# Performance work log

Measured on AMD Instinct MI355X. Metric: run time of the kernel, lower is better.

The kernel has to match this reference:

```python
import jax, jax.numpy as jnp
import numpy as np

B, C_IN, C_OUT, STYLE_DIM, H, W = 8, 512, 512, 512, 32, 32

def setup_inputs() -> dict:
    key = jax.random.key(0)
    k = jax.random.split(key, 7)
    x = jax.random.normal(k[0], (B, C_IN, H, W), dtype=jnp.float32)
    style = jax.random.normal(k[1], (B, STYLE_DIM), dtype=jnp.float32)
    noise = jax.random.normal(k[2], (B, 1, 2 * H, 2 * W), dtype=jnp.float32)
    # learned params (Conv2d weight, style_fc Linear, output bias)
    conv_w = jax.random.normal(k[3], (C_OUT, C_IN, 3, 3), dtype=jnp.float32) * 0.05
    fc_w = jax.random.normal(k[4], (C_IN, STYLE_DIM), dtype=jnp.float32) * 0.05
    fc_b = jax.random.normal(k[5], (C_IN,), dtype=jnp.float32) * 0.05
    bias = jnp.zeros((1, C_OUT, 1, 1), dtype=jnp.float32)
    return {"x": x, "style": style, "noise": noise,
            "conv_w": conv_w, "fc_w": fc_w, "fc_b": fc_b, "bias": bias}

def reference(x, style, noise, conv_w, fc_w, fc_b, bias):
    b, c, h, w = x.shape
    o = conv_w.shape[0]
    x = jnp.repeat(jnp.repeat(x, 2, axis=2), 2, axis=3)  # (B, C, 2H, 2W)
    # style modulation: (B, C)
    s = style @ fc_w.T + fc_b
    # per-sample modulated weight (B, O, C, 3, 3)
    wmod = conv_w[None] * (s[:, None, :, None, None] + 1.0)
    # demodulation
    d = jax.lax.rsqrt(jnp.sum(wmod * wmod, axis=(2, 3, 4)) + 1e-8)  # (B, O)
    wmod = wmod * d[:, :, None, None, None]
    # grouped conv: one group per batch sample
    xr = x.reshape(1, b * c, 2 * h, 2 * w)
    wr = wmod.reshape(b * o, c, 3, 3)
    y = jax.lax.conv_general_dilated(
        xr, wr, window_strides=(1, 1), padding='SAME',
        feature_group_count=b,
        dimension_numbers=('NCHW', 'OIHW', 'NCHW'))
    y = y.reshape(b, o, 2 * h, 2 * w) + bias + noise
    return jax.nn.leaky_relu(y, negative_slope=0.2)
```

## Files before the change

### kernel.cpp

```cpp
#include <hip/hip_runtime.h>

typedef short v8s __attribute__((ext_vector_type(8)));
typedef float f32x4 __attribute__((ext_vector_type(4)));
typedef unsigned short ushort_t;

#define BB    8
#define CIN   512
#define COUT  512
#define SDIM  512

static __device__ __forceinline__ ushort_t f2bf(float f) {
    union { float f; unsigned u; } un; un.f = f;
    unsigned r = un.u + 0x7FFF + ((un.u >> 16) & 1);
    return (ushort_t)(r >> 16);
}

__global__ void k_style(const float* __restrict__ style, const float* __restrict__ fc_w,
                        const float* __restrict__ fc_b, float* __restrict__ m) {
    __shared__ float sst[SDIM];
    const int b = blockIdx.y;
    for (int k = threadIdx.x; k < SDIM; k += 256) sst[k] = style[b * SDIM + k];
    __syncthreads();
    const int c = blockIdx.x * 256 + threadIdx.x;
    float acc = fc_b[c];
    const float* wr = fc_w + c * SDIM;
    for (int k = 0; k < SDIM; k += 4) {
        float4 w4 = *(const float4*)(wr + k);
        acc += w4.x * sst[k] + w4.y * sst[k + 1] + w4.z * sst[k + 2] + w4.w * sst[k + 3];
    }
    m[b * CIN + c] = acc + 1.0f;
}

__global__ void k_wprep(const float* __restrict__ conv_w, float* __restrict__ q,
                        ushort_t* __restrict__ Wb) {
    const int idx = blockIdx.x * 256 + threadIdx.x;
    if (idx >= COUT * CIN) return;
    const int o = idx >> 9, c = idx & 511;
    float w[3][3];
    const float* wp = conv_w + idx * 9;
    float qs = 0.f;
    for (int i = 0; i < 3; i++)
        for (int j = 0; j < 3; j++) {
            float v = wp[i * 3 + j];
            w[i][j] = v;
            qs += v * v;
        }
    q[idx] = qs;
    const int ch = c >> 5, kg = (c >> 3) & 3, c8 = c & 7;
    for (int py = 0; py < 2; py++) {
        float rs[2][3];
        for (int kx = 0; kx < 3; kx++) {
            rs[0][kx] = (py == 0) ? w[0][kx] : w[0][kx] + w[1][kx];
            rs[1][kx] = (py == 0) ? w[1][kx] + w[2][kx] : w[2][kx];
        }
        for (int px = 0; px < 2; px++) {
            const int p = py * 2 + px;
            float vals[4];
            if (px == 0) {
                vals[0] = rs[0][0];
                vals[1] = rs[0][1] + rs[0][2];
                vals[2] = rs[1][0];
                vals[3] = rs[1][1] + rs[1][2];
            } else {
                vals[0] = rs[0][0] + rs[0][1];
                vals[1] = rs[0][2];
                vals[2] = rs[1][0] + rs[1][1];
                vals[3] = rs[1][2];
            }
            for (int t = 0; t < 4; t++)
                Wb[(size_t)p * (16 * 4 * 4 * 512 * 8) + (size_t)ch * (4 * 4 * 512 * 8)
                   + ((size_t)(t * 4 + kg) * 512 + o) * 8 + c8] = f2bf(vals[t]);
        }
    }
}

__global__ void k_demod(const float* __restrict__ m, const float* __restrict__ q,
                        float* __restrict__ d) {
    const int w = (blockIdx.x * 256 + threadIdx.x) >> 6;
    const int L = threadIdx.x & 63;
    const int b = w >> 9, o = w & 511;
    float4 q1 = *(const float4*)(q + o * 512 + L * 8);
    float4 q2 = *(const float4*)(q + o * 512 + L * 8 + 4);
    float4 m1 = *(const float4*)(m + b * 512 + L * 8);
    float4 m2 = *(const float4*)(m + b * 512 + L * 8 + 4);
    float acc = m1.x * m1.x * q1.x + m1.y * m1.y * q1.y + m1.z * m1.z * q1.z +
                m1.w * m1.w * q1.w + m2.x * m2.x * q2.x + m2.y * m2.y * q2.y +
                m2.z * m2.z * q2.z + m2.w * m2.w * q2.w;
    for (int off = 32; off; off >>= 1) acc += __shfl_down(acc, off, 64);
    if (L == 0) d[w] = rsqrtf(acc + 1e-8f);
}

__global__ void k_xprep(const float* __restrict__ x, const float* __restrict__ m,
                        ushort_t* __restrict__ Xt) {
    __shared__ __align__(16) ushort_t lt[32 * 528];
    const int r = blockIdx.x, b = blockIdx.y, t = threadIdx.x;
    for (int s = t; s < 4096; s += 256) {
        const int c = s >> 3, q4 = (s & 7) * 4;
        float4 v = *(const float4*)(x + (((size_t)(b * CIN + c) * 32 + r) * 32 + q4));
        const float mv = m[b * CIN + c];
        lt[(q4 + 0) * 528 + c] = f2bf(v.x * mv);
        lt[(q4 + 1) * 528 + c] = f2bf(v.y * mv);
        lt[(q4 + 2) * 528 + c] = f2bf(v.z * mv);
        lt[(q4 + 3) * 528 + c] = f2bf(v.w * mv);
    }
    __syncthreads();
    for (int s = t; s < 2048; s += 256) {
        const int qq = s >> 6, c8 = s & 63;
        v8s v = *(v8s*)&lt[qq * 528 + c8 * 8];
        *(v8s*)(Xt + (((size_t)(b * 32 + r) * 32 + qq) * 512 + c8 * 8)) = v;
    }
}

#define KS 136

__global__ __launch_bounds__(256, 2) void k_gemm(
    const ushort_t* __restrict__ Xt, const ushort_t* __restrict__ Wb,
    const float* __restrict__ dmod, const float* __restrict__ bias,
    const float* __restrict__ noise, float* __restrict__ out) {
    __shared__ __align__(16) ushort_t Wt[128 * KS];
    __shared__ __align__(16) ushort_t Xs[128 * KS];

    const int tid = threadIdx.x;
    const int L = tid & 63, wid = tid >> 6;
    const int o0 = blockIdx.x * 128;
    const int r0 = blockIdx.y * 4;
    const int b = blockIdx.z >> 2, p = blockIdx.z & 3;
    const int py = p >> 1, px = p & 1;
    const int ry0 = py ? 0 : -1, cx0 = px ? 0 : -1;
    const int wo = (wid >> 1) * 64, wn = (wid & 1) * 64;
    const int l15 = L & 15, l4 = L >> 4;

    const ushort_t* XtB = Xt + (size_t)b * (32 * 32 * 512);
    const ushort_t* WbP = Wb + (size_t)p * (16 * 4 * 4 * 512 * 8);
    const v8s z8 = {0, 0, 0, 0, 0, 0, 0, 0};

    f32x4 acc[4][4];
#pragma unroll
    for (int i = 0; i < 4; i++)
#pragma unroll
        for (int j = 0; j < 4; j++) acc[i][j] = {0.f, 0.f, 0.f, 0.f};

    v8s rw[8], rx[8];

    auto loadc = [&](int c0) {
        const ushort_t* WbC = WbP + (size_t)(c0 >> 5) * (4 * 4 * 512 * 8);
#pragma unroll
        for (int i = 0; i < 8; i++) {
            const int slot = tid + i * 256;
            const int row = slot >> 4, t = (slot >> 2) & 3, cg = slot & 3;
            rw[i] = *(const v8s*)(WbC + ((size_t)((t * 4 + cg) * 512 + o0 + row)) * 8);
            const int gr = r0 + (row >> 5) + ry0 + (t >> 1);
            const int gq = (row & 31) + cx0 + (t & 1);
            v8s xv = z8;
            if ((unsigned)gr < 32u && (unsigned)gq < 32u)
                xv = *(const v8s*)(XtB + (size_t)((gr * 32 + gq) * 512 + c0 + cg * 8));
            rx[i] = xv;
        }
    };

    loadc(0);
    for (int c0 = 0; c0 < CIN; c0 += 32) {
        __syncthreads();
#pragma unroll
        for (int i = 0; i < 8; i++) {
            const int slot = tid + i * 256;
            const int row = slot >> 4, t = (slot >> 2) & 3, cg = slot & 3;
            const int ldso = row * KS + t * 32 + cg * 8;
            *(v8s*)&Wt[ldso] = rw[i];
            *(v8s*)&Xs[ldso] = rx[i];
        }
        __syncthreads();
        if (c0 + 32 < CIN) loadc(c0 + 32);
#pragma unroll
        for (int s = 0; s < 4; s++) {
            const int kb = s * 32 + l4 * 8;
            v8s af[4], bf[4];
#pragma unroll
            for (int i = 0; i < 4; i++)
                af[i] = *(const v8s*)&Wt[(wo + i * 16 + l15) * KS + kb];
#pragma unroll
            for (int j = 0; j < 4; j++)
                bf[j] = *(const v8s*)&Xs[(wn + j * 16 + l15) * KS + kb];
#pragma unroll
            for (int i = 0; i < 4; i++)
#pragma unroll
                for (int j = 0; j < 4; j++)
                    acc[i][j] = __builtin_amdgcn_mfma_f32_16x16x32_bf16(
                        af[i], bf[j], acc[i][j], 0, 0, 0);
        }
    }

    const float* db = dmod + b * COUT;
    float nz[4];
    int ooff[4];
#pragma unroll
    for (int j = 0; j < 4; j++) {
        const int n = wn + j * 16 + l15;
        const int Y = 2 * (r0 + (n >> 5)) + py, X = 2 * (n & 31) + px;
        nz[j] = noise[b * 4096 + Y * 64 + X];
        ooff[j] = Y * 64 + X;
    }
    float* outB = out + (size_t)b * COUT * 4096;
#pragma unroll
    for (int i = 0; i < 4; i++) {
        const int ob = o0 + wo + i * 16 + l4 * 4;
        float4 d4 = *(const float4*)(db + ob);
        float4 b4 = *(const float4*)(bias + ob);
        const float dv[4] = {d4.x, d4.y, d4.z, d4.w};
        const float bv[4] = {b4.x, b4.y, b4.z, b4.w};
#pragma unroll
        for (int reg = 0; reg < 4; reg++) {
            float* orow = outB + (size_t)(ob + reg) * 4096;
#pragma unroll
            for (int j = 0; j < 4; j++) {
                float v = acc[i][j][reg] * dv[reg] + bv[reg] + nz[j];
                orow[ooff[j]] = v > 0.f ? v : 0.2f * v;
            }
        }
    }
}

extern "C" void kernel_launch(void* const* d_in, const int* in_sizes, int n_in,
                              void* d_out, int out_size, void* d_ws, size_t ws_size,
                              hipStream_t stream) {
    const float* x      = (const float*)d_in[0];
    const float* style  = (const float*)d_in[1];
    const float* noise  = (const float*)d_in[2];
    const float* conv_w = (const float*)d_in[3];
    const float* fc_w   = (const float*)d_in[4];
    const float* fc_b   = (const float*)d_in[5];
    const float* bias   = (const float*)d_in[6];
    float* out = (float*)d_out;

    float* ws = (float*)d_ws;
    float* m    = ws;
    float* dmod = ws + 4096;
    float* q    = ws + 8192;
    ushort_t* XtU = (ushort_t*)(ws + 270336);
    ushort_t* WbU = XtU + 4194304;

    k_style<<<dim3(2, BB), 256, 0, stream>>>(style, fc_w, fc_b, m);
    k_wprep<<<(COUT * CIN + 255) / 256, 256, 0, stream>>>(conv_w, q, WbU);
    k_xprep<<<dim3(32, BB), 256, 0, stream>>>(x, m, XtU);
    k_demod<<<1024, 256, 0, stream>>>(m, q, dmod);
    k_gemm<<<dim3(4, 8, 32), 256, 0, stream>>>(XtU, WbU, dmod, bias, noise, out);
}
```

Measured before the change: 215.1 us.

## Merge prep kernels and double-buffer GEMM with direct global-to-LDS loads

Fuses the four preprocessing kernels into two launches, which removes launch overhead and serialization. The GEMM main loop now uses global_load_lds to copy tiles straight into double-buffered, XOR-swizzled LDS, replacing the register-staged single buffer and stepping K by 16 channels with one barrier per step. Out-of-range halo loads read from a zeroed guard buffer. Block indices are remapped to change the scheduling order across CUs. The new scheme depends on global_load_lds wave-slot layout semantics and adds more loop iterations.

```diff
diff --git a/kernel.cpp b/kernel.cpp
--- a/kernel.cpp
+++ b/kernel.cpp
@@ -9,122 +9,136 @@
 #define COUT  512
 #define SDIM  512
 
+#define GLDS(g, l)                                                      \
+    __builtin_amdgcn_global_load_lds(                                   \
+        (const __attribute__((address_space(1))) void*)(g),             \
+        (__attribute__((address_space(3))) void*)(l), 16, 0, 0)
+
 static __device__ __forceinline__ ushort_t f2bf(float f) {
     union { float f; unsigned u; } un; un.f = f;
     unsigned r = un.u + 0x7FFF + ((un.u >> 16) & 1);
     return (ushort_t)(r >> 16);
 }
 
-__global__ void k_style(const float* __restrict__ style, const float* __restrict__ fc_w,
-                        const float* __restrict__ fc_b, float* __restrict__ m) {
+__global__ void k_prep1(const float* __restrict__ style, const float* __restrict__ fc_w,
+                        const float* __restrict__ fc_b, float* __restrict__ m,
+                        const float* __restrict__ conv_w, float* __restrict__ q,
+                        ushort_t* __restrict__ Wb, float* __restrict__ guard) {
     __shared__ float sst[SDIM];
-    const int b = blockIdx.y;
-    for (int k = threadIdx.x; k < SDIM; k += 256) sst[k] = style[b * SDIM + k];
-    __syncthreads();
-    const int c = blockIdx.x * 256 + threadIdx.x;
-    float acc = fc_b[c];
-    const float* wr = fc_w + c * SDIM;
-    for (int k = 0; k < SDIM; k += 4) {
-        float4 w4 = *(const float4*)(wr + k);
-        acc += w4.x * sst[k] + w4.y * sst[k + 1] + w4.z * sst[k + 2] + w4.w * sst[k + 3];
-    }
-    m[b * CIN + c] = acc + 1.0f;
-}
-
-__global__ void k_wprep(const float* __restrict__ conv_w, float* __restrict__ q,
-                        ushort_t* __restrict__ Wb) {
-    const int idx = blockIdx.x * 256 + threadIdx.x;
-    if (idx >= COUT * CIN) return;
-    const int o = idx >> 9, c = idx & 511;
-    float w[3][3];
-    const float* wp = conv_w + idx * 9;
-    float qs = 0.f;
-    for (int i = 0; i < 3; i++)
-        for (int j = 0; j < 3; j++) {
-            float v = wp[i * 3 + j];
-            w[i][j] = v;
-            qs += v * v;
-        }
-    q[idx] = qs;
-    const int ch = c >> 5, kg = (c >> 3) & 3, c8 = c & 7;
-    for (int py = 0; py < 2; py++) {
-        float rs[2][3];
-        for (int kx = 0; kx < 3; kx++) {
-            rs[0][kx] = (py == 0) ? w[0][kx] : w[0][kx] + w[1][kx];
-            rs[1][kx] = (py == 0) ? w[1][kx] + w[2][kx] : w[2][kx];
-        }
-        for (int px = 0; px < 2; px++) {
-            const int p = py * 2 + px;
-            float vals[4];
-            if (px == 0) {
-                vals[0] = rs[0][0];
-                vals[1] = rs[0][1] + rs[0][2];
-                vals[2] = rs[1][0];
-                vals[3] = rs[1][1] + rs[1][2];
-            } else {
-                vals[0] = rs[0][0] + rs[0][1];
-                vals[1] = rs[0][2];
-                vals[2] = rs[1][0] + rs[1][1];
-                vals[3] = rs[1][2];
-            }
-            for (int t = 0; t < 4; t++)
-                Wb[(size_t)p * (16 * 4 * 4 * 512 * 8) + (size_t)ch * (4 * 4 * 512 * 8)
-                   + ((size_t)(t * 4 + kg) * 512 + o) * 8 + c8] = f2bf(vals[t]);
-        }
-    }
-}
-
-__global__ void k_demod(const float* __restrict__ m, const float* __restrict__ q,
+    const int bid = blockIdx.x;
+    if (bid < 1024) {
+        const int idx = bid * 256 + threadIdx.x;
+        const int o = idx >> 9, c = idx & 511;
+        float w[3][3];
+        const float* wp = conv_w + idx * 9;
+        float qs = 0.f;
+        for (int i = 0; i < 3; i++)
+            for (int j = 0; j < 3; j++) {
+                float v = wp[i * 3 + j];
+                w[i][j] = v;
+                qs += v * v;
+            }
+        q[idx] = qs;
+        const int ch = c >> 5, kg = (c >> 3) & 3, c8 = c & 7;
+        for (int py = 0; py < 2; py++) {
+            float rs[2][3];
+            for (int kx = 0; kx < 3; kx++) {
+                rs[0][kx] = (py == 0) ? w[0][kx] : w[0][kx] + w[1][kx];
+                rs[1][kx] = (py == 0) ? w[1][kx] + w[2][kx] : w[2][kx];
+            }
+            for (int px = 0; px < 2; px++) {
+                const int p = py * 2 + px;
+                float vals[4];
+                if (px == 0) {
+                    vals[0] = rs[0][0];
+                    vals[1] = rs[0][1] + rs[0][2];
+                    vals[2] = rs[1][0];
+                    vals[3] = rs[1][1] + rs[1][2];
+                } else {
+                    vals[0] = rs[0][0] + rs[0][1];
+                    vals[1] = rs[0][2];
+                    vals[2] = rs[1][0] + rs[1][1];
+                    vals[3] = rs[1][2];
+                }
+                for (int t = 0; t < 4; t++)
+                    Wb[(size_t)p * (16 * 4 * 4 * 512 * 8) + (size_t)ch * (4 * 4 * 512 * 8)
+                       + ((size_t)(t * 4 + kg) * 512 + o) * 8 + c8] = f2bf(vals[t]);
+            }
+        }
+    } else {
+        const int sb = bid - 1024;
+        const int bx = sb & 1, b = sb >> 1;
+        if (sb == 0 && threadIdx.x < 8) guard[threadIdx.x] = 0.f;
+        for (int k = threadIdx.x; k < SDIM; k += 256) sst[k] = style[b * SDIM + k];
+        __syncthreads();
+        const int c = bx * 256 + threadIdx.x;
+        float acc = fc_b[c];
+        const float* wr = fc_w + c * SDIM;
+        for (int k = 0; k < SDIM; k += 4) {
+            float4 w4 = *(const float4*)(wr + k);
+            acc += w4.x * sst[k] + w4.y * sst[k + 1] + w4.z * sst[k + 2] + w4.w * sst[k + 3];
+        }
+        m[b * CIN + c] = acc + 1.0f;
+    }
+}
+
+__global__ void k_prep2(const float* __restrict__ x, const float* __restrict__ m,
+                        ushort_t* __restrict__ Xt, const float* __restrict__ q,
                         float* __restrict__ d) {
-    const int w = (blockIdx.x * 256 + threadIdx.x) >> 6;
-    const int L = threadIdx.x & 63;
-    const int b = w >> 9, o = w & 511;
-    float4 q1 = *(const float4*)(q + o * 512 + L * 8);
-    float4 q2 = *(const float4*)(q + o * 512 + L * 8 + 4);
-    float4 m1 = *(const float4*)(m + b * 512 + L * 8);
-    float4 m2 = *(const float4*)(m + b * 512 + L * 8 + 4);
-    float acc = m1.x * m1.x * q1.x + m1.y * m1.y * q1.y + m1.z * m1.z * q1.z +
-                m1.w * m1.w * q1.w + m2.x * m2.x * q2.x + m2.y * m2.y * q2.y +
-                m2.z * m2.z * q2.z + m2.w * m2.w * q2.w;
-    for (int off = 32; off; off >>= 1) acc += __shfl_down(acc, off, 64);
-    if (L == 0) d[w] = rsqrtf(acc + 1e-8f);
-}
-
-__global__ void k_xprep(const float* __restrict__ x, const float* __restrict__ m,
-                        ushort_t* __restrict__ Xt) {
     __shared__ __align__(16) ushort_t lt[32 * 528];
-    const int r = blockIdx.x, b = blockIdx.y, t = threadIdx.x;
-    for (int s = t; s < 4096; s += 256) {
-        const int c = s >> 3, q4 = (s & 7) * 4;
-        float4 v = *(const float4*)(x + (((size_t)(b * CIN + c) * 32 + r) * 32 + q4));
-        const float mv = m[b * CIN + c];
-        lt[(q4 + 0) * 528 + c] = f2bf(v.x * mv);
-        lt[(q4 + 1) * 528 + c] = f2bf(v.y * mv);
-        lt[(q4 + 2) * 528 + c] = f2bf(v.z * mv);
-        lt[(q4 + 3) * 528 + c] = f2bf(v.w * mv);
-    }
-    __syncthreads();
-    for (int s = t; s < 2048; s += 256) {
-        const int qq = s >> 6, c8 = s & 63;
-        v8s v = *(v8s*)&lt[qq * 528 + c8 * 8];
-        *(v8s*)(Xt + (((size_t)(b * 32 + r) * 32 + qq) * 512 + c8 * 8)) = v;
-    }
-}
-
-#define KS 136
+    const int bid = blockIdx.x, t = threadIdx.x;
+    if (bid < 256) {
+        const int r = bid & 31, b = bid >> 5;
+        for (int s = t; s < 4096; s += 256) {
+            const int c = s >> 3, q4 = (s & 7) * 4;
+            float4 v = *(const float4*)(x + (((size_t)(b * CIN + c) * 32 + r) * 32 + q4));
+            const float mv = m[b * CIN + c];
+            lt[(q4 + 0) * 528 + c] = f2bf(v.x * mv);
+            lt[(q4 + 1) * 528 + c] = f2bf(v.y * mv);
+            lt[(q4 + 2) * 528 + c] = f2bf(v.z * mv);
+            lt[(q4 + 3) * 528 + c] = f2bf(v.w * mv);
+        }
+        __syncthreads();
+        for (int s = t; s < 2048; s += 256) {
+            const int qq = s >> 6, c8 = s & 63;
+            v8s v = *(v8s*)&lt[qq * 528 + c8 * 8];
+            *(v8s*)(Xt + (((size_t)(b * 32 + r) * 32 + qq) * 512 + c8 * 8)) = v;
+        }
+    } else {
+        const int w = (bid - 256) * 4 + (t >> 6);
+        const int L = t & 63;
+        const int b = w >> 9, o = w & 511;
+        float4 q1 = *(const float4*)(q + o * 512 + L * 8);
+        float4 q2 = *(const float4*)(q + o * 512 + L * 8 + 4);
+        float4 m1 = *(const float4*)(m + b * 512 + L * 8);
+        float4 m2 = *(const float4*)(m + b * 512 + L * 8 + 4);
+        float acc = m1.x * m1.x * q1.x + m1.y * m1.y * q1.y + m1.z * m1.z * q1.z +
+                    m1.w * m1.w * q1.w + m2.x * m2.x * q2.x + m2.y * m2.y * q2.y +
+                    m2.z * m2.z * q2.z + m2.w * m2.w * q2.w;
+        for (int off = 32; off; off >>= 1) acc += __shfl_down(acc, off, 64);
+        if (L == 0) d[w] = rsqrtf(acc + 1e-8f);
+    }
+}
 
 __global__ __launch_bounds__(256, 2) void k_gemm(
     const ushort_t* __restrict__ Xt, const ushort_t* __restrict__ Wb,
     const float* __restrict__ dmod, const float* __restrict__ bias,
-    const float* __restrict__ noise, float* __restrict__ out) {
-    __shared__ __align__(16) ushort_t Wt[128 * KS];
-    __shared__ __align__(16) ushort_t Xs[128 * KS];
+    const float* __restrict__ noise, float* __restrict__ out,
+    const float* __restrict__ guard) {
+    __shared__ __align__(16) ushort_t Wt[2][128 * 64];
+    __shared__ __align__(16) ushort_t Xs[2][128 * 64];
 
     const int tid = threadIdx.x;
-    const int L = tid & 63, wid = tid >> 6;
-    const int o0 = blockIdx.x * 128;
-    const int r0 = blockIdx.y * 4;
-    const int b = blockIdx.z >> 2, p = blockIdx.z & 3;
+    const int L = tid & 63;
+    const int wid = tid >> 6;
+
+    const int lin = blockIdx.x + 4 * blockIdx.y + 32 * blockIdx.z;
+    const int log = (lin & 7) * 128 + (lin >> 3);
+    const int o0 = (log & 3) * 128;
+    const int r0 = ((log >> 2) & 7) * 4;
+    const int zz = log >> 5;
+    const int b = zz >> 2, p = zz & 3;
+
     const int py = p >> 1, px = p & 1;
     const int ry0 = py ? 0 : -1, cx0 = px ? 0 : -1;
     const int wo = (wid >> 1) * 64, wn = (wid & 1) * 64;
@@ -132,7 +146,6 @@
 
     const ushort_t* XtB = Xt + (size_t)b * (32 * 32 * 512);
     const ushort_t* WbP = Wb + (size_t)p * (16 * 4 * 4 * 512 * 8);
-    const v8s z8 = {0, 0, 0, 0, 0, 0, 0, 0};
 
     f32x4 acc[4][4];
 #pragma unroll
@@ -140,54 +153,57 @@
 #pragma unroll
         for (int j = 0; j < 4; j++) acc[i][j] = {0.f, 0.f, 0.f, 0.f};
 
-    v8s rw[8], rx[8];
-
-    auto loadc = [&](int c0) {
-        const ushort_t* WbC = WbP + (size_t)(c0 >> 5) * (4 * 4 * 512 * 8);
-#pragma unroll
-        for (int i = 0; i < 8; i++) {
-            const int slot = tid + i * 256;
-            const int row = slot >> 4, t = (slot >> 2) & 3, cg = slot & 3;
-            rw[i] = *(const v8s*)(WbC + ((size_t)((t * 4 + cg) * 512 + o0 + row)) * 8);
-            const int gr = r0 + (row >> 5) + ry0 + (t >> 1);
-            const int gq = (row & 31) + cx0 + (t & 1);
-            v8s xv = z8;
-            if ((unsigned)gr < 32u && (unsigned)gq < 32u)
-                xv = *(const v8s*)(XtB + (size_t)((gr * 32 + gq) * 512 + c0 + cg * 8));
-            rx[i] = xv;
+    auto stage = [&](int c0, ushort_t* wbuf, ushort_t* xbuf) {
+#pragma unroll
+        for (int i = 0; i < 4; i++) {
+            const int slot0 = i * 256 + (tid & 192);
+            const int slot = i * 256 + tid;
+            const int row = slot >> 3;
+            const int k16 = (slot & 7) ^ (row & 7);
+            const int tp = k16 >> 1;
+            const int cg = c0 + (k16 & 1) * 8;
+            const ushort_t* wsrc =
+                WbP + (size_t)(cg >> 5) * (4 * 4 * 512 * 8)
+                + ((size_t)((tp * 4 + ((cg >> 3) & 3)) * 512 + o0 + row)) * 8;
+            GLDS(wsrc, wbuf + (size_t)slot0 * 8);
+            const int gr = r0 + (row >> 5) + ry0 + (tp >> 1);
+            const int gq = (row & 31) + cx0 + (tp & 1);
+            const ushort_t* xsrc =
+                ((unsigned)gr < 32u && (unsigned)gq < 32u)
+                    ? XtB + (size_t)((gr * 32 + gq) * 512 + cg)
+                    : (const ushort_t*)guard;
+            GLDS(xsrc, xbuf + (size_t)slot0 * 8);
         }
     };
 
-    loadc(0);
-    for (int c0 = 0; c0 < CIN; c0 += 32) {
-        __syncthreads();
-#pragma unroll
-        for (int i = 0; i < 8; i++) {
-            const int slot = tid + i * 256;
-            const int row = slot >> 4, t = (slot >> 2) & 3, cg = slot & 3;
-            const int ldso = row * KS + t * 32 + cg * 8;
-            *(v8s*)&Wt[ldso] = rw[i];
-            *(v8s*)&Xs[ldso] = rx[i];
-        }
-        __syncthreads();
-        if (c0 + 32 < CIN) loadc(c0 + 32);
-#pragma unroll
-        for (int s = 0; s < 4; s++) {
-            const int kb = s * 32 + l4 * 8;
-            v8s af[4], bf[4];
+    stage(0, Wt[0], Xs[0]);
+    __syncthreads();
+
+    const int swz = (l15 & 7) << 3;
+    int cur = 0;
+    for (int c0 = 0; c0 < CIN; c0 += 16) {
+        if (c0 + 16 < CIN) stage(c0 + 16, Wt[cur ^ 1], Xs[cur ^ 1]);
+        const ushort_t* wbuf = Wt[cur];
+        const ushort_t* xbuf = Xs[cur];
+#pragma unroll
+        for (int s = 0; s < 2; s++) {
+            const int ko = (s * 32 + l4 * 8) ^ swz;
+            v8s af[4], bfr[4];
 #pragma unroll
             for (int i = 0; i < 4; i++)
-                af[i] = *(const v8s*)&Wt[(wo + i * 16 + l15) * KS + kb];
+                af[i] = *(const v8s*)&wbuf[(wo + i * 16 + l15) * 64 + ko];
 #pragma unroll
             for (int j = 0; j < 4; j++)
-                bf[j] = *(const v8s*)&Xs[(wn + j * 16 + l15) * KS + kb];
+                bfr[j] = *(const v8s*)&xbuf[(wn + j * 16 + l15) * 64 + ko];
 #pragma unroll
             for (int i = 0; i < 4; i++)
 #pragma unroll
                 for (int j = 0; j < 4; j++)
                     acc[i][j] = __builtin_amdgcn_mfma_f32_16x16x32_bf16(
-                        af[i], bf[j], acc[i][j], 0, 0, 0);
-        }
+                        af[i], bfr[j], acc[i][j], 0, 0, 0);
+        }
+        __syncthreads();
+        cur ^= 1;
     }
 
     const float* db = dmod + b * COUT;
@@ -233,15 +249,14 @@
     float* out = (float*)d_out;
 
     float* ws = (float*)d_ws;
-    float* m    = ws;
-    float* dmod = ws + 4096;
-    float* q    = ws + 8192;
-    ushort_t* XtU = (ushort_t*)(ws + 270336);
+    float* m     = ws;
+    float* dmod  = ws + 4096;
+    float* q     = ws + 8192;
+    float* guard = ws + 270336;
+    ushort_t* XtU = (ushort_t*)(ws + 270352);
     ushort_t* WbU = XtU + 4194304;
 
-    k_style<<<dim3(2, BB), 256, 0, stream>>>(style, fc_w, fc_b, m);
-    k_wprep<<<(COUT * CIN + 255) / 256, 256, 0, stream>>>(conv_w, q, WbU);
-    k_xprep<<<dim3(32, BB), 256, 0, stream>>>(x, m, XtU);
-    k_demod<<<1024, 256, 0, stream>>>(m, q, dmod);
-    k_gemm<<<dim3(4, 8, 32), 256, 0, stream>>>(XtU, WbU, dmod, bias, noise, out);
-}
+    k_prep1<<<1040, 256, 0, stream>>>(style, fc_w, fc_b, m, conv_w, q, WbU, guard);
+    k_prep2<<<1280, 256, 0, stream>>>(x, m, XtU, q, dmod);
+    k_gemm<<<dim3(4, 8, 32), 256, 0, stream>>>(XtU, WbU, dmod, bias, noise, out, guard);
+}
```

Measured after the change: 226.6 us. 1.05x slower.
